# Kernel optimization log

Measured on AMD Instinct MI355X. Metric: run time of the kernel, lower is better.

## Reference

```python
import jax, jax.numpy as jnp
import numpy as np

N_NODES = 50000
N_EDGES = 800000
IN_DIM = 128
EMB_DIM = 128
NUM_LAYER = 3
NUM_GRAPHS = 512
BN_EPS = 1e-5


def setup_inputs() -> dict:
    key = jax.random.key(0)
    ks = jax.random.split(key, 10)
    x = jax.random.normal(ks[0], (N_NODES, IN_DIM), jnp.float32)
    edge_index = jax.random.randint(ks[1], (2, N_EDGES), 0, N_NODES)
    batch = jnp.sort(jax.random.randint(ks[2], (N_NODES,), 0, NUM_GRAPHS))
    W = jax.random.normal(ks[3], (NUM_LAYER, EMB_DIM, EMB_DIM), jnp.float32) / np.sqrt(EMB_DIM)
    b_hidden = 0.01 * jax.random.normal(ks[4], (NUM_LAYER - 1, EMB_DIM), jnp.float32)
    bn_gamma = 1.0 + 0.1 * jax.random.normal(ks[5], (NUM_LAYER, EMB_DIM), jnp.float32)
    bn_beta = 0.1 * jax.random.normal(ks[6], (NUM_LAYER, EMB_DIM), jnp.float32)
    bn_mean = 0.1 * jax.random.normal(ks[7], (NUM_LAYER, EMB_DIM), jnp.float32)
    bn_var = jnp.ones((NUM_LAYER, EMB_DIM), jnp.float32)
    We = jax.random.normal(ks[8], (2 * EMB_DIM, 1), jnp.float32) / np.sqrt(2 * EMB_DIM)
    be = jnp.zeros((1,), jnp.float32)
    Wn = jax.random.normal(ks[9], (EMB_DIM, 1), jnp.float32) / np.sqrt(EMB_DIM)
    bn_bias = jnp.zeros((1,), jnp.float32)
    return dict(x=x, edge_index=edge_index, batch=batch, num_graphs=NUM_GRAPHS,
                W=W, b_hidden=b_hidden, bn_gamma=bn_gamma, bn_beta=bn_beta,
                bn_mean=bn_mean, bn_var=bn_var, We=We, be=be, Wn=Wn, bn_bias=bn_bias)


def batch_norm(x, gamma, beta, mean, var):
    # eval-mode BatchNorm1d with running stats
    return (x - mean) * jax.lax.rsqrt(var + BN_EPS) * gamma + beta


def gcn_propagate(h, edge_index, num_nodes):
    # symmetric-normalized GCN aggregation with self loops (edge_weight = 1)
    loop = jnp.arange(num_nodes)
    row = jnp.concatenate([edge_index[0], loop])
    col = jnp.concatenate([edge_index[1], loop])
    deg = jax.ops.segment_sum(jnp.ones(row.shape[0], h.dtype), row, num_segments=num_nodes)
    dis = jnp.where(deg > 0, jax.lax.rsqrt(jnp.maximum(deg, 1.0)), 0.0)
    norm = dis[row] * dis[col]  # [E+N]
    return jax.ops.segment_sum(norm[:, None] * h[row], col, num_segments=num_nodes)


def reg_mask(mask, seg, size):
    # mask: [S,1]; seg: [S] int segment ids; size graphs
    key_num = jax.ops.segment_sum(mask, seg, num_segments=size) + 1e-8
    env_num = jax.ops.segment_sum(1.0 - mask, seg, num_segments=size) + 1e-8
    non_zero = jax.ops.segment_sum((mask > 0).astype(jnp.float32), seg, num_segments=size)
    all_mask = jax.ops.segment_sum(jnp.ones_like(mask), seg, num_segments=size)
    return key_num, env_num, non_zero / all_mask


def _forward(x, W, b_hidden, bn_gamma, bn_beta, bn_mean, bn_var, We, be, Wn, bn_bias,
             edge_index, batch, num_graphs):
    N = x.shape[0]
    # layer 1: GCNConv(gfn=True) => BN then plain linear (no bias, no propagation)
    h = batch_norm(x, bn_gamma[0], bn_beta[0], bn_mean[0], bn_var[0]) @ W[0]
    h = jax.nn.relu(h)  # num_layer > 1; dropout is identity in eval
    n_hidden = W.shape[0] - 1
    for i in range(n_hidden):
        hb = batch_norm(h, bn_gamma[i + 1], bn_beta[i + 1], bn_mean[i + 1], bn_var[i + 1])
        h = gcn_propagate(hb @ W[i + 1], edge_index, N) + b_hidden[i]
        if i != n_hidden - 1:
            h = jax.nn.relu(h)
    node_rep = h  # [N, emb]

    row, col = edge_index[0], edge_index[1]
    D = node_rep.shape[1]
    node_key = jax.nn.sigmoid(node_rep @ Wn + bn_bias)  # [N,1]
    # cat([rep[row], rep[col]]) @ We == rep[row] @ We[:D] + rep[col] @ We[D:]
    edge_key = jax.nn.sigmoid(node_rep[row] @ We[:D] + node_rep[col] @ We[D:] + be)  # [E,1]

    node_key_num, node_env_num, nz_node_ratio = reg_mask(node_key, batch, num_graphs)
    edge_key_num, edge_env_num, nz_edge_ratio = reg_mask(edge_key, batch[row], num_graphs)
    return (node_key, edge_key, node_key_num, node_env_num,
            edge_key_num, edge_env_num, nz_node_ratio, nz_edge_ratio)


def reference(x, edge_index, batch, num_graphs, W, b_hidden, bn_gamma, bn_beta,
              bn_mean, bn_var, We, be, Wn, bn_bias):
    return _forward(x, W, b_hidden, bn_gamma, bn_beta, bn_mean, bn_var,
                    We, be, Wn, bn_bias, edge_index, batch, num_graphs)
```

## Files before the change

kernel.cpp:

```cpp
#include <hip/hip_runtime.h>
#include <cstddef>
#include <cstring>

#define NN 50000
#define NNP 50048
#define NE 800000
#define D 128
#define NG 512
#define BN_EPS 1e-5f
#define RSZC 25000
#define RSZF 12500
#define NCHUNK 64
#define CSZ 12500
#define EDGE_BLOCKS 256

typedef __bf16 bf16_t;
typedef __bf16 bf16x8 __attribute__((ext_vector_type(8)));
typedef float f32x4 __attribute__((ext_vector_type(4)));

#define OFF_ACCN 0
#define OFF_ACCE 2048
#define OFF_CTR  4096
#define ZERO_FLOATS 4160
#define OFF_DIS  4160
#define OFF_CNT  54208
#define OFF_COLP 104256
#define OFF_ENDS 154304
#define OFF_BSUM 204352
#define OFF_T1   204800
#define OFF_T2   254848
#define OFF_BP   304896
#define OFF_WPT  305408
#define OFF_PR   329984
#define OFF_PC   3533056
#define OFF_SRCS OFF_PR
#define OFF_HBFA 7536128
#define OFF_HBFB 10739200

#define O_NKEY 0
#define O_EKEY 50000
#define O_NKN  850000
#define O_NEN  850512
#define O_EKN  851024
#define O_EEN  851536
#define O_NZN  852048
#define O_NZE  852560

__device__ __forceinline__ float sigmoidf(float x) {
    return 1.0f / (1.0f + expf(-x));
}

__device__ __forceinline__ unsigned short f2bf_bits(float f) {
    bf16_t h = (bf16_t)f;
    unsigned short u;
    __builtin_memcpy(&u, &h, 2);
    return u;
}

__device__ __forceinline__ float bf_lo(unsigned int u) {
    return __uint_as_float(u << 16);
}
__device__ __forceinline__ float bf_hi(unsigned int u) {
    return __uint_as_float(u & 0xFFFF0000u);
}

__global__ __launch_bounds__(256) void count_prep(const int* __restrict__ ei,
                                                  int* __restrict__ PR,
                                                  int* __restrict__ PC,
                                                  const float* __restrict__ W,
                                                  const float* __restrict__ gamma,
                                                  const float* __restrict__ beta,
                                                  const float* __restrict__ mean,
                                                  const float* __restrict__ var,
                                                  bf16_t* __restrict__ Wpt,
                                                  float* __restrict__ bp) {
    const int tid = threadIdx.x;
    if (blockIdx.z == 2) {
        if (blockIdx.x == 0 && blockIdx.y < 3 && tid < D) {
            int l = blockIdx.y;
            int j = tid;
            float acc = 0.f;
            for (int k = 0; k < D; ++k) {
                float a = gamma[l * D + k] * rsqrtf(var[l * D + k] + BN_EPS);
                float c = beta[l * D + k] - mean[l * D + k] * a;
                float w = W[l * D * D + k * D + j];
                Wpt[l * D * D + j * D + k] = (bf16_t)(a * w);
                acc = fmaf(c, w, acc);
            }
            bp[l * D + j] = acc;
        }
        return;
    }
    extern __shared__ int hist[];
    const int r = blockIdx.x, p = blockIdx.y, dirz = blockIdx.z;
    for (int i = tid; i < RSZC; i += 256) hist[i] = 0;
    __syncthreads();
    const int base = r * RSZC;
    const int4* ids = (const int4*)(ei + dirz * NE + p * CSZ);
    for (int i = tid; i < CSZ / 4; i += 256) {
        int4 v = ids[i];
        int d0 = v.x - base, d1 = v.y - base, d2 = v.z - base, d3 = v.w - base;
        if ((unsigned)d0 < RSZC) atomicAdd(&hist[d0], 1);
        if ((unsigned)d1 < RSZC) atomicAdd(&hist[d1], 1);
        if ((unsigned)d2 < RSZC) atomicAdd(&hist[d2], 1);
        if ((unsigned)d3 < RSZC) atomicAdd(&hist[d3], 1);
    }
    __syncthreads();
    int* dst = (dirz == 0 ? PR : PC) + p * NNP + base;
    for (int i = tid; i < RSZC; i += 256) dst[i] = hist[i];
}

__global__ void csr_mid(const int* __restrict__ PR, int* __restrict__ PC,
                        float* __restrict__ dis, int* __restrict__ cnt,
                        int* __restrict__ colp, int* __restrict__ bsum) {
    __shared__ int s[256];
    int t = threadIdx.x;
    int i = blockIdx.x * 256 + t;
    int run = 0;
    if (i < NN) {
        int dg = 0;
#pragma unroll 8
        for (int k = 0; k < NCHUNK; ++k) dg += PR[k * NNP + i];
        dis[i] = rsqrtf((float)(dg + 1));
        for (int k = 0; k < NCHUNK; ++k) {
            int v = PC[k * NNP + i];
            PC[k * NNP + i] = run;
            run += v;
        }
        cnt[i] = run;
    }
    s[t] = run;
    __syncthreads();
    for (int o = 1; o < 256; o <<= 1) {
        int add = (t >= o) ? s[t - o] : 0;
        __syncthreads();
        s[t] += add;
        __syncthreads();
    }
    if (i < NN) colp[i] = s[t] - run;
    if (t == 255) bsum[blockIdx.x] = s[255];
}

__global__ void scan3(int* __restrict__ colp, const int* __restrict__ bsum,
                      const int* __restrict__ cnt, int* __restrict__ ends) {
    __shared__ int s[256];
    int t = threadIdx.x;
    int bid = blockIdx.x;
    s[t] = (t < bid) ? bsum[t] : 0;
    __syncthreads();
    for (int o = 128; o; o >>= 1) {
        if (t < o) s[t] += s[t + o];
        __syncthreads();
    }
    int boff = s[0];
    int i = bid * 256 + t;
    if (i < NN) {
        int v = colp[i] + boff;
        colp[i] = v;
        ends[i] = v + cnt[i];
    }
}

__global__ __launch_bounds__(256) void fill_part(const int* __restrict__ ei,
                                                 const int* __restrict__ colp,
                                                 const int* __restrict__ CPS,
                                                 const float* __restrict__ dis,
                                                 unsigned int* __restrict__ srcs) {
    __shared__ int curs[RSZF];
    const int r = blockIdx.x, p = blockIdx.y;
    const int tid = threadIdx.x;
    const int base = r * RSZF;
    for (int i = tid; i < RSZF; i += 256)
        curs[i] = colp[base + i] + CPS[p * NNP + base + i];
    __syncthreads();
    const int4* rows = (const int4*)(ei + p * CSZ);
    const int4* cols = (const int4*)(ei + NE + p * CSZ);
    for (int i = tid; i < CSZ / 4; i += 256) {
        int4 rv = rows[i];
        int4 cv = cols[i];
        int d;
        d = cv.x - base;
        if ((unsigned)d < RSZF)
            srcs[atomicAdd(&curs[d], 1)] =
                (unsigned int)rv.x | ((unsigned int)f2bf_bits(dis[rv.x]) << 16);
        d = cv.y - base;
        if ((unsigned)d < RSZF)
            srcs[atomicAdd(&curs[d], 1)] =
                (unsigned int)rv.y | ((unsigned int)f2bf_bits(dis[rv.y]) << 16);
        d = cv.z - base;
        if ((unsigned)d < RSZF)
            srcs[atomicAdd(&curs[d], 1)] =
                (unsigned int)rv.z | ((unsigned int)f2bf_bits(dis[rv.z]) << 16);
        d = cv.w - base;
        if ((unsigned)d < RSZF)
            srcs[atomicAdd(&curs[d], 1)] =
                (unsigned int)rv.w | ((unsigned int)f2bf_bits(dis[rv.w]) << 16);
    }
}

__global__ __launch_bounds__(256) void gemm01(const float* __restrict__ X,
                                              const bf16_t* __restrict__ Bt0,
                                              const bf16_t* __restrict__ Bt1,
                                              const float* __restrict__ bias0,
                                              const float* __restrict__ bias1,
                                              bf16_t* __restrict__ out) {
    extern __shared__ __align__(16) unsigned short smem[];
    unsigned short* Bs0 = smem;
    unsigned short* Bs1 = smem + 16384;
    unsigned short* As  = smem + 32768;
    const int tid = threadIdx.x;
    const int wv = tid >> 6;
    const int lane = tid & 63;
    const int l15 = lane & 15;
    const int l4 = lane >> 4;
    const int row0 = blockIdx.x * 64;

    for (int q = tid; q < 2048; q += 256) {
        int r = q >> 4, u = q & 15;
        int us = (u ^ (r & 7)) * 8;
        *(uint4*)&Bs0[r * 128 + us] = *(const uint4*)(Bt0 + r * D + u * 8);
        *(uint4*)&Bs1[r * 128 + us] = *(const uint4*)(Bt1 + r * D + u * 8);
    }

    bf16x8 afrag[4];
    {
        int r = row0 + wv * 16 + l15;
        int rc = (r < NN) ? r : (NN - 1);
#pragma unroll
        for (int kk = 0; kk < 4; ++kk) {
            int off = rc * D + kk * 32 + l4 * 8;
            float4 f0 = *(const float4*)(X + off);
            float4 f1 = *(const float4*)(X + off + 4);
            bf16x8 a;
            a[0] = (bf16_t)f0.x; a[1] = (bf16_t)f0.y;
            a[2] = (bf16_t)f0.z; a[3] = (bf16_t)f0.w;
            a[4] = (bf16_t)f1.x; a[5] = (bf16_t)f1.y;
            a[6] = (bf16_t)f1.z; a[7] = (bf16_t)f1.w;
            afrag[kk] = a;
        }
    }
    __syncthreads();

    const int rsw = l15 & 7;
    f32x4 acc[8];
#pragma unroll
    for (int n = 0; n < 8; ++n) acc[n] = (f32x4){0.f, 0.f, 0.f, 0.f};
#pragma unroll
    for (int n = 0; n < 8; ++n) {
#pragma unroll
        for (int kk = 0; kk < 4; ++kk) {
            bf16x8 bfrag = *(const bf16x8*)&Bs0[(n * 16 + l15) * 128 + ((kk * 4 + l4) ^ rsw) * 8];
            acc[n] = __builtin_amdgcn_mfma_f32_16x16x32_bf16(afrag[kk], bfrag, acc[n], 0, 0, 0);
        }
    }
#pragma unroll
    for (int n = 0; n < 8; ++n) {
        int col = n * 16 + l15;
        float bv = bias0[col];
#pragma unroll
        for (int r = 0; r < 4; ++r) {
            int rl = wv * 16 + l4 * 4 + r;
            float v = fmaxf(acc[n][r] + bv, 0.f);
            int cs = ((col >> 3) ^ (rl & 7));
            As[rl * 128 + cs * 8 + (col & 7)] = f2bf_bits(v);
        }
    }
    __syncthreads();

    const int rl = wv * 16 + l15;
    bf16x8 af2[4];
#pragma unroll
    for (int kk = 0; kk < 4; ++kk) {
        int cs = (kk * 4 + l4) ^ (rl & 7);
        af2[kk] = *(const bf16x8*)&As[rl * 128 + cs * 8];
    }
#pragma unroll
    for (int n = 0; n < 8; ++n) acc[n] = (f32x4){0.f, 0.f, 0.f, 0.f};
#pragma unroll
    for (int n = 0; n < 8; ++n) {
#pragma unroll
        for (int kk = 0; kk < 4; ++kk) {
            bf16x8 bfrag = *(const bf16x8*)&Bs1[(n * 16 + l15) * 128 + ((kk * 4 + l4) ^ rsw) * 8];
            acc[n] = __builtin_amdgcn_mfma_f32_16x16x32_bf16(af2[kk], bfrag, acc[n], 0, 0, 0);
        }
    }
#pragma unroll
    for (int n = 0; n < 8; ++n) {
        int col = n * 16 + l15;
        float bv = bias1[col];
#pragma unroll
        for (int r = 0; r < 4; ++r) {
            int row = row0 + wv * 16 + l4 * 4 + r;
            if (row < NN) out[(size_t)row * D + col] = (bf16_t)(acc[n][r] + bv);
        }
    }
}

__global__ __launch_bounds__(256) void gemm2(const bf16_t* __restrict__ A,
                                             const bf16_t* __restrict__ Bt,
                                             const float* __restrict__ bias,
                                             bf16_t* __restrict__ out) {
    __shared__ __align__(16) unsigned short Bs[128 * 128];
    const int tid = threadIdx.x;
    const int wv = tid >> 6;
    const int lane = tid & 63;
    const int l15 = lane & 15;
    const int l4 = lane >> 4;
    const int row0 = blockIdx.x * 64 + wv * 16;

    for (int q = tid; q < 2048; q += 256) {
        int r = q >> 4, u = q & 15;
        *(uint4*)&Bs[r * 128 + (u ^ (r & 7)) * 8] = *(const uint4*)(Bt + r * D + u * 8);
    }

    bf16x8 afrag[4];
    {
        int r = row0 + l15;
        int rc = (r < NN) ? r : (NN - 1);
#pragma unroll
        for (int kk = 0; kk < 4; ++kk)
            afrag[kk] = *(const bf16x8*)(A + rc * D + kk * 32 + l4 * 8);
    }
    __syncthreads();

    const int rsw = l15 & 7;
    f32x4 acc[8];
#pragma unroll
    for (int n = 0; n < 8; ++n) acc[n] = (f32x4){0.f, 0.f, 0.f, 0.f};
#pragma unroll
    for (int n = 0; n < 8; ++n) {
#pragma unroll
        for (int kk = 0; kk < 4; ++kk) {
            bf16x8 bfrag = *(const bf16x8*)&Bs[(n * 16 + l15) * 128 + ((kk * 4 + l4) ^ rsw) * 8];
            acc[n] = __builtin_amdgcn_mfma_f32_16x16x32_bf16(afrag[kk], bfrag, acc[n], 0, 0, 0);
        }
    }
#pragma unroll
    for (int n = 0; n < 8; ++n) {
        int col = n * 16 + l15;
        float bv = bias[col];
#pragma unroll
        for (int r = 0; r < 4; ++r) {
            int row = row0 + l4 * 4 + r;
            if (row < NN) out[(size_t)row * D + col] = (bf16_t)(acc[n][r] + bv);
        }
    }
}

template <int POST>
__global__ __launch_bounds__(256) void prop_gather(
    const int* __restrict__ colp, const int* __restrict__ ends,
    const unsigned int* __restrict__ srcs, const float* __restrict__ dis,
    const bf16_t* __restrict__ hin, bf16_t* __restrict__ hout,
    const float* __restrict__ bias) {
    int n = blockIdx.x * 4 + (threadIdx.x >> 6);
    n = __builtin_amdgcn_readfirstlane(n);
    int lane = threadIdx.x & 63;
    if (n >= NN) return;
    const int start = colp[n];
    const int end = ends[n];
    const float dn = dis[n];
    unsigned int u = ((const unsigned int*)(hin + (size_t)n * D))[lane];
    float ax = dn * bf_lo(u), ay = dn * bf_hi(u);
    int i = start;
    for (; i + 3 < end; i += 4) {
        unsigned int e0 = srcs[i], e1 = srcs[i + 1], e2 = srcs[i + 2], e3 = srcs[i + 3];
        unsigned int u0 = ((const unsigned int*)(hin + (size_t)(e0 & 0xFFFFu) * D))[lane];
        unsigned int u1 = ((const unsigned int*)(hin + (size_t)(e1 & 0xFFFFu) * D))[lane];
        unsigned int u2 = ((const unsigned int*)(hin + (size_t)(e2 & 0xFFFFu) * D))[lane];
        unsigned int u3 = ((const unsigned int*)(hin + (size_t)(e3 & 0xFFFFu) * D))[lane];
        float w0 = bf_hi(e0), w1 = bf_hi(e1), w2 = bf_hi(e2), w3 = bf_hi(e3);
        ax = fmaf(w0, bf_lo(u0), ax); ay = fmaf(w0, bf_hi(u0), ay);
        ax = fmaf(w1, bf_lo(u1), ax); ay = fmaf(w1, bf_hi(u1), ay);
        ax = fmaf(w2, bf_lo(u2), ax); ay = fmaf(w2, bf_hi(u2), ay);
        ax = fmaf(w3, bf_lo(u3), ax); ay = fmaf(w3, bf_hi(u3), ay);
    }
    for (; i < end; ++i) {
        unsigned int e0 = srcs[i];
        unsigned int u0 = ((const unsigned int*)(hin + (size_t)(e0 & 0xFFFFu) * D))[lane];
        float w0 = bf_hi(e0);
        ax = fmaf(w0, bf_lo(u0), ax); ay = fmaf(w0, bf_hi(u0), ay);
    }
    float vx = dn * ax, vy = dn * ay;
    if (POST == 0) {
        float2 bb = ((const float2*)bias)[lane];
        vx = fmaxf(vx + bb.x, 0.f);
        vy = fmaxf(vy + bb.y, 0.f);
    }
    unsigned int pk = (unsigned int)f2bf_bits(vx) | ((unsigned int)f2bf_bits(vy) << 16);
    ((unsigned int*)(hout + (size_t)n * D))[lane] = pk;
}

__global__ __launch_bounds__(256) void node_kernel(
    const bf16_t* __restrict__ h, const float* __restrict__ bh1,
    const float* __restrict__ We, const float* __restrict__ Wn,
    const float* __restrict__ bnb, const int* __restrict__ batch,
    float* __restrict__ nkey_out, float* __restrict__ t1, float* __restrict__ t2,
    float* __restrict__ accN) {
    __shared__ float binK[NG], binE[NG], binZ[NG], binC[NG];
    const int tid = threadIdx.x;
    for (int i = tid; i < NG; i += 256) { binK[i] = 0.f; binE[i] = 0.f; binZ[i] = 0.f; binC[i] = 0.f; }
    __syncthreads();

    const int CHUNK = 98;
    int start = blockIdx.x * CHUNK;
    int end = min(start + CHUNK, NN);
    int sub = tid >> 5;
    int l32 = tid & 31;
    float bnb0 = bnb[0];

    float4 w1 = ((const float4*)We)[l32];
    float4 w2 = ((const float4*)(We + D))[l32];
    float4 wn = ((const float4*)Wn)[l32];
    float4 bb = ((const float4*)bh1)[l32];

    for (int n = start + sub; n < end; n += 8) {
        uint2 pk = ((const uint2*)(h + (size_t)n * D))[l32];
        float v0 = bf_lo(pk.x) + bb.x;
        float v1 = bf_hi(pk.x) + bb.y;
        float v2 = bf_lo(pk.y) + bb.z;
        float v3 = bf_hi(pk.y) + bb.w;
        float s1 = v0 * w1.x + v1 * w1.y + v2 * w1.z + v3 * w1.w;
        float s2 = v0 * w2.x + v1 * w2.y + v2 * w2.z + v3 * w2.w;
        float s3 = v0 * wn.x + v1 * wn.y + v2 * wn.z + v3 * wn.w;
        for (int o = 16; o; o >>= 1) {
            s1 += __shfl_xor(s1, o);
            s2 += __shfl_xor(s2, o);
            s3 += __shfl_xor(s3, o);
        }
        if (l32 == 0) {
            t1[n] = s1;
            t2[n] = s2;
            float nk = sigmoidf(s3 + bnb0);
            nkey_out[n] = nk;
            int g = batch[n];
            atomicAdd(&binK[g], nk);
            atomicAdd(&binE[g], 1.0f - nk);
            if (nk > 0.f) atomicAdd(&binZ[g], 1.0f);
            atomicAdd(&binC[g], 1.0f);
        }
    }
    __syncthreads();
    if (start < NN) {
        int glo = batch[start];
        int ghi = batch[end - 1];
        for (int g = glo + tid; g <= ghi; g += 256) {
            unsafeAtomicAdd(&accN[g], binK[g]);
            unsafeAtomicAdd(&accN[NG + g], binE[g]);
            unsafeAtomicAdd(&accN[2 * NG + g], binZ[g]);
            unsafeAtomicAdd(&accN[3 * NG + g], binC[g]);
        }
    }
}

__global__ __launch_bounds__(256) void edge_final(
    const int* __restrict__ ei, const float* __restrict__ t1,
    const float* __restrict__ t2, const float* __restrict__ be,
    const int* __restrict__ batch, float* __restrict__ ekey_out,
    float* __restrict__ accE, const float* __restrict__ accN,
    int* __restrict__ ctr, float* __restrict__ out) {
    __shared__ float binK[NG], binE[NG], binZ[NG], binC[NG];
    __shared__ int isLast;
    const int tid = threadIdx.x;
    for (int i = tid; i < NG; i += 256) { binK[i] = 0.f; binE[i] = 0.f; binZ[i] = 0.f; binC[i] = 0.f; }
    __syncthreads();
    float be0 = be[0];
    int stride4 = gridDim.x * 256;
    for (int q = blockIdx.x * 256 + tid; q < NE / 4; q += stride4) {
        int4 r4 = ((const int4*)ei)[q];
        int4 c4 = ((const int4*)(ei + NE))[q];
        float a0 = t1[r4.x], a1 = t1[r4.y], a2 = t1[r4.z], a3 = t1[r4.w];
        float b0 = t2[c4.x], b1 = t2[c4.y], b2 = t2[c4.z], b3 = t2[c4.w];
        int g0 = batch[r4.x], g1 = batch[r4.y], g2 = batch[r4.z], g3 = batch[r4.w];
        float e0 = sigmoidf(a0 + b0 + be0);
        float e1 = sigmoidf(a1 + b1 + be0);
        float e2 = sigmoidf(a2 + b2 + be0);
        float e3 = sigmoidf(a3 + b3 + be0);
        ((float4*)ekey_out)[q] = make_float4(e0, e1, e2, e3);
        atomicAdd(&binK[g0], e0); atomicAdd(&binE[g0], 1.0f - e0);
        if (e0 > 0.f) atomicAdd(&binZ[g0], 1.0f);
        atomicAdd(&binC[g0], 1.0f);
        atomicAdd(&binK[g1], e1); atomicAdd(&binE[g1], 1.0f - e1);
        if (e1 > 0.f) atomicAdd(&binZ[g1], 1.0f);
        atomicAdd(&binC[g1], 1.0f);
        atomicAdd(&binK[g2], e2); atomicAdd(&binE[g2], 1.0f - e2);
        if (e2 > 0.f) atomicAdd(&binZ[g2], 1.0f);
        atomicAdd(&binC[g2], 1.0f);
        atomicAdd(&binK[g3], e3); atomicAdd(&binE[g3], 1.0f - e3);
        if (e3 > 0.f) atomicAdd(&binZ[g3], 1.0f);
        atomicAdd(&binC[g3], 1.0f);
    }
    __syncthreads();
    for (int g = tid; g < NG; g += 256) {
        if (binC[g] != 0.f) {
            unsafeAtomicAdd(&accE[g], binK[g]);
            unsafeAtomicAdd(&accE[NG + g], binE[g]);
            unsafeAtomicAdd(&accE[2 * NG + g], binZ[g]);
            unsafeAtomicAdd(&accE[3 * NG + g], binC[g]);
        }
    }
    __syncthreads();
    if (tid == 0) {
        __threadfence();
        int old = atomicAdd(ctr, 1);
        isLast = (old == (int)gridDim.x - 1);
    }
    __syncthreads();
    if (isLast) {
        __threadfence();
        for (int g = tid; g < NG; g += 256) {
            out[O_NKN + g] = accN[g] + 1e-8f;
            out[O_NEN + g] = accN[NG + g] + 1e-8f;
            out[O_EKN + g] = accE[g] + 1e-8f;
            out[O_EEN + g] = accE[NG + g] + 1e-8f;
            out[O_NZN + g] = accN[2 * NG + g] / accN[3 * NG + g];
            out[O_NZE + g] = accE[2 * NG + g] / accE[3 * NG + g];
        }
    }
}

extern "C" void kernel_launch(void* const* d_in, const int* in_sizes, int n_in,
                              void* d_out, int out_size, void* d_ws, size_t ws_size,
                              hipStream_t stream) {
    const float* x     = (const float*)d_in[0];
    const int*   ei    = (const int*)d_in[1];
    const int*   batch = (const int*)d_in[2];
    const float* W     = (const float*)d_in[4];
    const float* bh    = (const float*)d_in[5];
    const float* gamma = (const float*)d_in[6];
    const float* beta  = (const float*)d_in[7];
    const float* mean  = (const float*)d_in[8];
    const float* var   = (const float*)d_in[9];
    const float* We    = (const float*)d_in[10];
    const float* be    = (const float*)d_in[11];
    const float* Wn    = (const float*)d_in[12];
    const float* bnb   = (const float*)d_in[13];

    float* ws  = (float*)d_ws;
    float* out = (float*)d_out;

    float*        accN = ws + OFF_ACCN;
    float*        accE = ws + OFF_ACCE;
    int*          ctr  = (int*)(ws + OFF_CTR);
    float*        dis  = ws + OFF_DIS;
    int*          cnt  = (int*)(ws + OFF_CNT);
    int*          colp = (int*)(ws + OFF_COLP);
    int*          ends = (int*)(ws + OFF_ENDS);
    int*          bsum = (int*)(ws + OFF_BSUM);
    float*        t1   = ws + OFF_T1;
    float*        t2   = ws + OFF_T2;
    float*        bp   = ws + OFF_BP;
    bf16_t*       Wpt  = (bf16_t*)(ws + OFF_WPT);
    int*          PR   = (int*)(ws + OFF_PR);
    int*          PC   = (int*)(ws + OFF_PC);
    unsigned int* srcs = (unsigned int*)(ws + OFF_SRCS);
    bf16_t*       hbfA = (bf16_t*)(ws + OFF_HBFA);
    bf16_t*       hbfB = (bf16_t*)(ws + OFF_HBFB);

    hipMemsetAsync(d_ws, 0, (size_t)ZERO_FLOATS * sizeof(float), stream);

    count_prep<<<dim3(2, NCHUNK, 3), 256, RSZC * sizeof(int), stream>>>(
        ei, PR, PC, W, gamma, beta, mean, var, Wpt, bp);
    const int NB = (NN + 255) / 256;
    csr_mid<<<NB, 256, 0, stream>>>(PR, PC, dis, cnt, colp, bsum);
    scan3<<<NB, 256, 0, stream>>>(colp, bsum, cnt, ends);
    fill_part<<<dim3(4, NCHUNK), 256, 0, stream>>>(ei, colp, PC, dis, srcs);

    const int GB = (NN + 63) / 64;
    gemm01<<<GB, 256, 81920, stream>>>(x, Wpt, Wpt + D * D, bp, bp + D, hbfB);
    prop_gather<0><<<12500, 256, 0, stream>>>(colp, ends, srcs, dis, hbfB, hbfA, bh);
    gemm2<<<GB, 256, 0, stream>>>(hbfA, Wpt + 2 * D * D, bp + 2 * D, hbfB);
    prop_gather<1><<<12500, 256, 0, stream>>>(colp, ends, srcs, dis, hbfB, hbfA, nullptr);

    node_kernel<<<512, 256, 0, stream>>>(hbfA, bh + D, We, Wn, bnb, batch,
                                         out + O_NKEY, t1, t2, accN);
    edge_final<<<EDGE_BLOCKS, 256, 0, stream>>>(ei, t1, t2, be, batch,
                                                out + O_EKEY, accE, accN, ctr, out);
}
```

Before: 214.6 us.

## Fuse CSR scan kernels, split gather by feature half, pack edge-final tables

Merges csr_mid and scan3 into one kernel that uses a grid-wide atomic counter with a spin-wait to combine block sums, removing one launch. The propagation gather now uses 32 lanes per node per feature half, with blocks interleaved so both halves of a node run close together, which changes the gather's access pattern. node_kernel writes t1, t2 and the graph id into one float4 table so edge_final does one 16-byte gather per endpoint instead of three scalar gathers. The spin-wait depends on every block of the scan being resident at the same time, and the float4 table reads more bytes per edge.

Measured after the change: 252.1 us. +17.5%, slower.

```diff
diff --git a/kernel.cpp b/kernel.cpp
--- a/kernel.cpp
+++ b/kernel.cpp
@@ -21,19 +21,19 @@
 #define OFF_ACCN 0
 #define OFF_ACCE 2048
 #define OFF_CTR  4096
+#define OFF_CTR2 4104
 #define ZERO_FLOATS 4160
 #define OFF_DIS  4160
 #define OFF_CNT  54208
 #define OFF_COLP 104256
 #define OFF_ENDS 154304
 #define OFF_BSUM 204352
-#define OFF_T1   204800
-#define OFF_T2   254848
 #define OFF_BP   304896
 #define OFF_WPT  305408
 #define OFF_PR   329984
 #define OFF_PC   3533056
 #define OFF_SRCS OFF_PR
+#define OFF_TB   1129984
 #define OFF_HBFA 7536128
 #define OFF_HBFB 10739200
 
@@ -110,12 +110,13 @@
     for (int i = tid; i < RSZC; i += 256) dst[i] = hist[i];
 }
 
-__global__ void csr_mid(const int* __restrict__ PR, int* __restrict__ PC,
-                        float* __restrict__ dis, int* __restrict__ cnt,
-                        int* __restrict__ colp, int* __restrict__ bsum) {
+__global__ void csr_mid_scan(const int* __restrict__ PR, int* __restrict__ PC,
+                             float* __restrict__ dis, int* __restrict__ cnt,
+                             int* __restrict__ colp, int* __restrict__ bsum,
+                             int* __restrict__ ends, int* __restrict__ ctr2) {
     __shared__ int s[256];
-    int t = threadIdx.x;
-    int i = blockIdx.x * 256 + t;
+    const int t = threadIdx.x;
+    const int i = blockIdx.x * 256 + t;
     int run = 0;
     if (i < NN) {
         int dg = 0;
@@ -137,27 +138,32 @@
         s[t] += add;
         __syncthreads();
     }
-    if (i < NN) colp[i] = s[t] - run;
-    if (t == 255) bsum[blockIdx.x] = s[255];
-}
-
-__global__ void scan3(int* __restrict__ colp, const int* __restrict__ bsum,
-                      const int* __restrict__ cnt, int* __restrict__ ends) {
-    __shared__ int s[256];
-    int t = threadIdx.x;
-    int bid = blockIdx.x;
-    s[t] = (t < bid) ? bsum[t] : 0;
+    const int local_excl = s[t] - run;
+    if (t == 255) {
+        __hip_atomic_store(&bsum[blockIdx.x], s[255], __ATOMIC_RELEASE,
+                           __HIP_MEMORY_SCOPE_AGENT);
+        __hip_atomic_fetch_add(ctr2, 1, __ATOMIC_RELEASE, __HIP_MEMORY_SCOPE_AGENT);
+    }
+    if (t == 0) {
+        while (__hip_atomic_load(ctr2, __ATOMIC_ACQUIRE, __HIP_MEMORY_SCOPE_AGENT) <
+               (int)gridDim.x) {
+            __builtin_amdgcn_s_sleep(8);
+        }
+    }
+    __syncthreads();
+    s[t] = (t < blockIdx.x)
+               ? __hip_atomic_load(&bsum[t], __ATOMIC_ACQUIRE, __HIP_MEMORY_SCOPE_AGENT)
+               : 0;
     __syncthreads();
     for (int o = 128; o; o >>= 1) {
         if (t < o) s[t] += s[t + o];
         __syncthreads();
     }
-    int boff = s[0];
-    int i = bid * 256 + t;
+    const int boff = s[0];
     if (i < NN) {
-        int v = colp[i] + boff;
+        int v = local_excl + boff;
         colp[i] = v;
-        ends[i] = v + cnt[i];
+        ends[i] = v + run;
     }
 }
 
@@ -348,27 +354,31 @@
 }
 
 template <int POST>
-__global__ __launch_bounds__(256) void prop_gather(
+__global__ __launch_bounds__(256) void prop_half(
     const int* __restrict__ colp, const int* __restrict__ ends,
     const unsigned int* __restrict__ srcs, const float* __restrict__ dis,
     const bf16_t* __restrict__ hin, bf16_t* __restrict__ hout,
     const float* __restrict__ bias) {
-    int n = blockIdx.x * 4 + (threadIdx.x >> 6);
-    n = __builtin_amdgcn_readfirstlane(n);
-    int lane = threadIdx.x & 63;
+    const int b = blockIdx.x;
+    const int half = (b & 7) >> 2;
+    const int ord = (b >> 3) * 4 + (b & 3);
+    const int sub = threadIdx.x >> 5;
+    const int l32 = threadIdx.x & 31;
+    const int n = ord * 8 + sub;
     if (n >= NN) return;
     const int start = colp[n];
     const int end = ends[n];
     const float dn = dis[n];
-    unsigned int u = ((const unsigned int*)(hin + (size_t)n * D))[lane];
+    const unsigned int* hinh = (const unsigned int*)(hin + half * 64);
+    unsigned int u = hinh[(size_t)n * 64 + l32];
     float ax = dn * bf_lo(u), ay = dn * bf_hi(u);
     int i = start;
     for (; i + 3 < end; i += 4) {
         unsigned int e0 = srcs[i], e1 = srcs[i + 1], e2 = srcs[i + 2], e3 = srcs[i + 3];
-        unsigned int u0 = ((const unsigned int*)(hin + (size_t)(e0 & 0xFFFFu) * D))[lane];
-        unsigned int u1 = ((const unsigned int*)(hin + (size_t)(e1 & 0xFFFFu) * D))[lane];
-        unsigned int u2 = ((const unsigned int*)(hin + (size_t)(e2 & 0xFFFFu) * D))[lane];
-        unsigned int u3 = ((const unsigned int*)(hin + (size_t)(e3 & 0xFFFFu) * D))[lane];
+        unsigned int u0 = hinh[(size_t)(e0 & 0xFFFFu) * 64 + l32];
+        unsigned int u1 = hinh[(size_t)(e1 & 0xFFFFu) * 64 + l32];
+        unsigned int u2 = hinh[(size_t)(e2 & 0xFFFFu) * 64 + l32];
+        unsigned int u3 = hinh[(size_t)(e3 & 0xFFFFu) * 64 + l32];
         float w0 = bf_hi(e0), w1 = bf_hi(e1), w2 = bf_hi(e2), w3 = bf_hi(e3);
         ax = fmaf(w0, bf_lo(u0), ax); ay = fmaf(w0, bf_hi(u0), ay);
         ax = fmaf(w1, bf_lo(u1), ax); ay = fmaf(w1, bf_hi(u1), ay);
@@ -377,25 +387,25 @@
     }
     for (; i < end; ++i) {
         unsigned int e0 = srcs[i];
-        unsigned int u0 = ((const unsigned int*)(hin + (size_t)(e0 & 0xFFFFu) * D))[lane];
+        unsigned int u0 = hinh[(size_t)(e0 & 0xFFFFu) * 64 + l32];
         float w0 = bf_hi(e0);
         ax = fmaf(w0, bf_lo(u0), ax); ay = fmaf(w0, bf_hi(u0), ay);
     }
     float vx = dn * ax, vy = dn * ay;
     if (POST == 0) {
-        float2 bb = ((const float2*)bias)[lane];
+        float2 bb = ((const float2*)bias)[half * 32 + l32];
         vx = fmaxf(vx + bb.x, 0.f);
         vy = fmaxf(vy + bb.y, 0.f);
     }
     unsigned int pk = (unsigned int)f2bf_bits(vx) | ((unsigned int)f2bf_bits(vy) << 16);
-    ((unsigned int*)(hout + (size_t)n * D))[lane] = pk;
+    ((unsigned int*)(hout + (size_t)n * D + half * 64))[l32] = pk;
 }
 
 __global__ __launch_bounds__(256) void node_kernel(
     const bf16_t* __restrict__ h, const float* __restrict__ bh1,
     const float* __restrict__ We, const float* __restrict__ Wn,
     const float* __restrict__ bnb, const int* __restrict__ batch,
-    float* __restrict__ nkey_out, float* __restrict__ t1, float* __restrict__ t2,
+    float* __restrict__ nkey_out, float4* __restrict__ tb,
     float* __restrict__ accN) {
     __shared__ float binK[NG], binE[NG], binZ[NG], binC[NG];
     const int tid = threadIdx.x;
@@ -429,11 +439,10 @@
             s3 += __shfl_xor(s3, o);
         }
         if (l32 == 0) {
-            t1[n] = s1;
-            t2[n] = s2;
             float nk = sigmoidf(s3 + bnb0);
             nkey_out[n] = nk;
             int g = batch[n];
+            tb[n] = make_float4(s1, s2, __int_as_float(g), 0.f);
             atomicAdd(&binK[g], nk);
             atomicAdd(&binE[g], 1.0f - nk);
             if (nk > 0.f) atomicAdd(&binZ[g], 1.0f);
@@ -454,9 +463,8 @@
 }
 
 __global__ __launch_bounds__(256) void edge_final(
-    const int* __restrict__ ei, const float* __restrict__ t1,
-    const float* __restrict__ t2, const float* __restrict__ be,
-    const int* __restrict__ batch, float* __restrict__ ekey_out,
+    const int* __restrict__ ei, const float4* __restrict__ tb,
+    const float* __restrict__ be, float* __restrict__ ekey_out,
     float* __restrict__ accE, const float* __restrict__ accN,
     int* __restrict__ ctr, float* __restrict__ out) {
     __shared__ float binK[NG], binE[NG], binZ[NG], binC[NG];
@@ -469,13 +477,14 @@
     for (int q = blockIdx.x * 256 + tid; q < NE / 4; q += stride4) {
         int4 r4 = ((const int4*)ei)[q];
         int4 c4 = ((const int4*)(ei + NE))[q];
-        float a0 = t1[r4.x], a1 = t1[r4.y], a2 = t1[r4.z], a3 = t1[r4.w];
-        float b0 = t2[c4.x], b1 = t2[c4.y], b2 = t2[c4.z], b3 = t2[c4.w];
-        int g0 = batch[r4.x], g1 = batch[r4.y], g2 = batch[r4.z], g3 = batch[r4.w];
-        float e0 = sigmoidf(a0 + b0 + be0);
-        float e1 = sigmoidf(a1 + b1 + be0);
-        float e2 = sigmoidf(a2 + b2 + be0);
-        float e3 = sigmoidf(a3 + b3 + be0);
+        float4 tr0 = tb[r4.x], tr1 = tb[r4.y], tr2 = tb[r4.z], tr3 = tb[r4.w];
+        float4 tc0 = tb[c4.x], tc1 = tb[c4.y], tc2 = tb[c4.z], tc3 = tb[c4.w];
+        int g0 = __float_as_int(tr0.z), g1 = __float_as_int(tr1.z);
+        int g2 = __float_as_int(tr2.z), g3 = __float_as_int(tr3.z);
+        float e0 = sigmoidf(tr0.x + tc0.y + be0);
+        float e1 = sigmoidf(tr1.x + tc1.y + be0);
+        float e2 = sigmoidf(tr2.x + tc2.y + be0);
+        float e3 = sigmoidf(tr3.x + tc3.y + be0);
         ((float4*)ekey_out)[q] = make_float4(e0, e1, e2, e3);
         atomicAdd(&binK[g0], e0); atomicAdd(&binE[g0], 1.0f - e0);
         if (e0 > 0.f) atomicAdd(&binZ[g0], 1.0f);
@@ -542,18 +551,18 @@
     float*        accN = ws + OFF_ACCN;
     float*        accE = ws + OFF_ACCE;
     int*          ctr  = (int*)(ws + OFF_CTR);
+    int*          ctr2 = (int*)(ws + OFF_CTR2);
     float*        dis  = ws + OFF_DIS;
     int*          cnt  = (int*)(ws + OFF_CNT);
     int*          colp = (int*)(ws + OFF_COLP);
     int*          ends = (int*)(ws + OFF_ENDS);
     int*          bsum = (int*)(ws + OFF_BSUM);
-    float*        t1   = ws + OFF_T1;
-    float*        t2   = ws + OFF_T2;
     float*        bp   = ws + OFF_BP;
     bf16_t*       Wpt  = (bf16_t*)(ws + OFF_WPT);
     int*          PR   = (int*)(ws + OFF_PR);
     int*          PC   = (int*)(ws + OFF_PC);
     unsigned int* srcs = (unsigned int*)(ws + OFF_SRCS);
+    float4*       tb   = (float4*)(ws + OFF_TB);
     bf16_t*       hbfA = (bf16_t*)(ws + OFF_HBFA);
     bf16_t*       hbfB = (bf16_t*)(ws + OFF_HBFB);
 
@@ -562,18 +571,17 @@
     count_prep<<<dim3(2, NCHUNK, 3), 256, RSZC * sizeof(int), stream>>>(
         ei, PR, PC, W, gamma, beta, mean, var, Wpt, bp);
     const int NB = (NN + 255) / 256;
-    csr_mid<<<NB, 256, 0, stream>>>(PR, PC, dis, cnt, colp, bsum);
-    scan3<<<NB, 256, 0, stream>>>(colp, bsum, cnt, ends);
+    csr_mid_scan<<<NB, 256, 0, stream>>>(PR, PC, dis, cnt, colp, bsum, ends, ctr2);
     fill_part<<<dim3(4, NCHUNK), 256, 0, stream>>>(ei, colp, PC, dis, srcs);
 
     const int GB = (NN + 63) / 64;
     gemm01<<<GB, 256, 81920, stream>>>(x, Wpt, Wpt + D * D, bp, bp + D, hbfB);
-    prop_gather<0><<<12500, 256, 0, stream>>>(colp, ends, srcs, dis, hbfB, hbfA, bh);
+    prop_half<0><<<12504, 256, 0, stream>>>(colp, ends, srcs, dis, hbfB, hbfA, bh);
     gemm2<<<GB, 256, 0, stream>>>(hbfA, Wpt + 2 * D * D, bp + 2 * D, hbfB);
-    prop_gather<1><<<12500, 256, 0, stream>>>(colp, ends, srcs, dis, hbfB, hbfA, nullptr);
+    prop_half<1><<<12504, 256, 0, stream>>>(colp, ends, srcs, dis, hbfB, hbfA, nullptr);
 
     node_kernel<<<512, 256, 0, stream>>>(hbfA, bh + D, We, Wn, bnb, batch,
-                                         out + O_NKEY, t1, t2, accN);
-    edge_final<<<EDGE_BLOCKS, 256, 0, stream>>>(ei, t1, t2, be, batch,
-                                                out + O_EKEY, accE, accN, ctr, out);
-}
+                                         out + O_NKEY, tb, accN);
+    edge_final<<<EDGE_BLOCKS, 256, 0, stream>>>(ei, tb, be, out + O_EKEY,
+                                                accE, accN, ctr, out);
+}
```
